# Kernel optimization log

Hardware: AMD Instinct MI355X
Metric: run time of the kernel (lower is better)

The kernel has to match this reference:

```python
import jax, jax.numpy as jnp
import numpy as np

H = 16        # attn_num
A = 64        # head dim
W = 512       # sliding-window length (ar_attn_window_len)
THETA = 10000.0
EPS = 1e-6    # norm_eps


def _rope(x):
    # x: [b, h, s, a]
    s, a = x.shape[2], x.shape[3]
    inv_freq = (1.0 / THETA) ** (jnp.arange(0, a, 2, dtype=jnp.float32) / a)
    freqs = jnp.arange(s, dtype=jnp.float32)[:, None] * inv_freq[None, :]  # [s, a/2]
    cos, sin = jnp.cos(freqs), jnp.sin(freqs)
    x1, x2 = jnp.split(x, 2, axis=-1)
    return jnp.concatenate([x1 * cos + x2 * sin, -x1 * sin + x2 * cos], axis=-1)


def _l2_normalize(x):
    # F.normalize(x, dim=-1, eps): x / max(||x||_2, eps)
    n = jnp.sqrt(jnp.sum(x * x, axis=-1, keepdims=True))
    return x / jnp.maximum(n, EPS)


def setup_inputs() -> dict:
    key = jax.random.key(0)
    kq, kk, kv = jax.random.split(key, 3)
    b, s, d = 2, 4096, H * A
    return {
        "xq": jax.random.normal(kq, (b, s, d), dtype=jnp.float32),
        "xk": jax.random.normal(kk, (b, s, d), dtype=jnp.float32),
        "xv": jax.random.normal(kv, (b, s, d), dtype=jnp.float32),
    }


def reference(xq, xk, xv):
    b, s, d = xq.shape
    to_heads = lambda x: x.reshape(b, s, H, A).transpose(0, 2, 1, 3)  # b h s a
    q, k, v = to_heads(xq), to_heads(xk), to_heads(xv)

    # qk-norm then RoPE, exactly as Attention.forward
    q = _rope(_l2_normalize(q))
    k = _rope(_l2_normalize(k))

    # Block-banded causal sliding-window attention (honors the block sparsity):
    # query block i attends only to key blocks i-1 and i (window = block size W).
    nb = s // W
    qb = q.reshape(b, H, nb, W, A)

    def band(x):
        xb = x.reshape(b, H, nb, W, A)
        xp = jnp.pad(xb, ((0, 0), (0, 0), (1, 0), (0, 0), (0, 0)))  # zero block in front
        return jnp.concatenate([xp[:, :, :-1], xp[:, :, 1:]], axis=3)  # [b,H,nb,2W,A]

    kb, vb = band(k), band(v)

    scale = 1.0 / np.sqrt(A)
    scores = jnp.einsum("bhnqa,bhnka->bhnqk", qb, kb) * scale  # [b,H,nb,W,2W]

    # mask: causal (q >= kv), window (q - kv < W), and kv index in range (>= 0)
    r = jnp.arange(W)
    c = jnp.arange(2 * W)
    diff = r[:, None] - (c[None, :] - W)               # q_global - kv_global
    within = (diff >= 0) & (diff < W)                   # [W, 2W]
    kv_global = (jnp.arange(nb)[:, None] - 1) * W + c[None, :]  # [nb, 2W]
    mask = within[None, :, :] & (kv_global[:, None, :] >= 0)    # [nb, W, 2W]

    scores = jnp.where(mask[None, None], scores, -1e30)
    p = jax.nn.softmax(scores, axis=-1)
    out = jnp.einsum("bhnqk,bhnka->bhnqa", p, vb)       # [b,H,nb,W,A]
    out = out.reshape(b, H, s, A).transpose(0, 2, 1, 3).reshape(b, s, d)
    return out
```

## Files before the change

### kernel.cpp

```cpp
#include <hip/hip_runtime.h>

#define NB 2
#define NH 16
#define SEQ 4096
#define HD 64
#define DIM 1024
#define WIN 512

typedef float f32x16 __attribute__((ext_vector_type(16)));
typedef short bf16x8 __attribute__((ext_vector_type(8)));
typedef unsigned int u32x4 __attribute__((ext_vector_type(4)));
typedef unsigned int u32x2 __attribute__((ext_vector_type(2)));
typedef unsigned short u16;
typedef unsigned int u32;

__device__ __forceinline__ u16 f2bf(float x) {
    u32 u = __float_as_uint(x);
    u += 0x7FFFu + ((u >> 16) & 1u);
    return (u16)(u >> 16);
}

__device__ __forceinline__ u32 cvtpk(float lo, float hi) {
    u32 r;
    asm("v_cvt_pk_bf16_f32 %0, %1, %2" : "=v"(r) : "v"(lo), "v"(hi));
    return r;
}

__device__ __forceinline__ float pexp2(float x) {
    return 1.f + x * (0.69314718f + x * (0.24022651f + x * 0.05550411f));
}

__global__ void trig_kernel(float* __restrict__ ct, float* __restrict__ st) {
    int idx = blockIdx.x * 256 + threadIdx.x;
    int s = idx >> 5, j = idx & 31;
    float inv = powf(1.0f / 10000.0f, (float)j * (1.0f / 32.0f));
    float ang = (float)s * inv;
    ct[idx] = cosf(ang);
    st[idx] = sinf(ang);
}

__device__ __forceinline__ void norm_rope_row(const float* __restrict__ row,
                                              const float* __restrict__ cr,
                                              const float* __restrict__ sr,
                                              float scale, u16* __restrict__ dst, int a) {
    float4 u0 = *(const float4*)(row + 8 * a);
    float4 u1 = *(const float4*)(row + 8 * a + 4);
    float4 v0 = *(const float4*)(row + 32 + 8 * a);
    float4 v1 = *(const float4*)(row + 32 + 8 * a + 4);
    float x1[8] = {u0.x, u0.y, u0.z, u0.w, u1.x, u1.y, u1.z, u1.w};
    float x2[8] = {v0.x, v0.y, v0.z, v0.w, v1.x, v1.y, v1.z, v1.w};
    float ss = 0.f;
#pragma unroll
    for (int i = 0; i < 8; ++i) ss += x1[i] * x1[i] + x2[i] * x2[i];
    ss += __shfl_xor(ss, 1);
    ss += __shfl_xor(ss, 2);
    float rn = scale / fmaxf(sqrtf(ss), 1e-6f);
    u16 o1[8], o2[8];
#pragma unroll
    for (int i = 0; i < 8; ++i) {
        float c = cr[8 * a + i], sn = sr[8 * a + i];
        o1[i] = f2bf((x1[i] * c + x2[i] * sn) * rn);
        o2[i] = f2bf((x2[i] * c - x1[i] * sn) * rn);
    }
    uint4 w1, w2;
    w1.x = (u32)o1[0] | ((u32)o1[1] << 16); w1.y = (u32)o1[2] | ((u32)o1[3] << 16);
    w1.z = (u32)o1[4] | ((u32)o1[5] << 16); w1.w = (u32)o1[6] | ((u32)o1[7] << 16);
    w2.x = (u32)o2[0] | ((u32)o2[1] << 16); w2.y = (u32)o2[2] | ((u32)o2[3] << 16);
    w2.z = (u32)o2[4] | ((u32)o2[5] << 16); w2.w = (u32)o2[6] | ((u32)o2[7] << 16);
    *(uint4*)(dst + 8 * a) = w1;
    *(uint4*)(dst + 32 + 8 * a) = w2;
}

__global__ void k_prep(const float* __restrict__ xk,
                       const float* __restrict__ ctab, const float* __restrict__ stab,
                       u16* __restrict__ Kn) {
    int bid = blockIdx.x;
    int bh = bid >> 6, stile = bid & 63;
    int b = bh >> 4, h = bh & 15;
    int t = threadIdx.x;
    int lr = t >> 2, a = t & 3;
    int s = stile * 64 + lr;
    size_t inoff = ((size_t)(b * SEQ + s)) * DIM + h * HD;
    size_t outoff = ((size_t)bh * SEQ + s) * HD;
    norm_rope_row(xk + inoff, ctab + (size_t)s * 32, stab + (size_t)s * 32, 1.0f, Kn + outoff, a);
}

__global__ void v_prep(const float* __restrict__ xv, u16* __restrict__ Vt) {
    __shared__ u16 tile[64][66];
    int bid = blockIdx.x;
    int bh = bid >> 6, stile = bid & 63;
    int b = bh >> 4, h = bh & 15;
    int t = threadIdx.x;
    int lr = t >> 2, a = t & 3;
    int s = stile * 64 + lr;
    const float* vrow = xv + ((size_t)(b * SEQ + s)) * DIM + h * HD + 16 * a;
#pragma unroll
    for (int c = 0; c < 4; ++c) {
        float4 w = *(const float4*)(vrow + 4 * c);
        tile[lr][16 * a + 4 * c + 0] = f2bf(w.x);
        tile[lr][16 * a + 4 * c + 1] = f2bf(w.y);
        tile[lr][16 * a + 4 * c + 2] = f2bf(w.z);
        tile[lr][16 * a + 4 * c + 3] = f2bf(w.w);
    }
    __syncthreads();
    int d = t >> 2;
    u32 pk[8];
#pragma unroll
    for (int i = 0; i < 8; ++i) {
        u16 lo = tile[16 * a + 2 * i][d];
        u16 hi = tile[16 * a + 2 * i + 1][d];
        pk[i] = (u32)lo | ((u32)hi << 16);
    }
    u16* dst = Vt + ((size_t)bh * HD + d) * SEQ + stile * 64 + 16 * a;
    *(uint4*)(dst) = make_uint4(pk[0], pk[1], pk[2], pk[3]);
    *(uint4*)(dst + 8) = make_uint4(pk[4], pk[5], pk[6], pk[7]);
}

#define KROW 72
#define VROW 40
__global__ __launch_bounds__(256, 4) void attn_kernel(const float* __restrict__ xq,
                                                      const u16* __restrict__ Kn,
                                                      const u16* __restrict__ Vt,
                                                      const float* __restrict__ ctab,
                                                      const float* __restrict__ stab,
                                                      float* __restrict__ out) {
    __shared__ __align__(16) u16 Kl[2][32 * KROW];
    __shared__ __align__(16) u16 Vl[2][64 * VROW];
    int phys = blockIdx.x;
    int logical = (phys & 7) * 128 + (phys >> 3);
    int bh = logical >> 5, qt = logical & 31;
    int b = bh >> 4, h = bh & 15;
    int tid = threadIdx.x;
    int w = tid >> 6, l = tid & 63;
    int q = l & 31, hi = l >> 5;
    int qblk = qt * 128;
    int qw0 = qblk + w * 32;
    const u16* Kh = Kn + (size_t)bh * SEQ * HD;
    const u16* Vh = Vt + (size_t)bh * HD * SEQ;
    int dq = qw0 + q;

    const float* qrow = xq + ((size_t)(b * SEQ + dq)) * DIM + h * HD;
    float4 xa0 = *(const float4*)(qrow + hi * 8);
    float4 xa1 = *(const float4*)(qrow + hi * 8 + 4);
    float4 xb0 = *(const float4*)(qrow + 16 + hi * 8);
    float4 xb1 = *(const float4*)(qrow + 16 + hi * 8 + 4);
    float4 ya0 = *(const float4*)(qrow + 32 + hi * 8);
    float4 ya1 = *(const float4*)(qrow + 36 + hi * 8);
    float4 yb0 = *(const float4*)(qrow + 48 + hi * 8);
    float4 yb1 = *(const float4*)(qrow + 52 + hi * 8);
    auto d4 = [](float4 v) { return v.x * v.x + v.y * v.y + v.z * v.z + v.w * v.w; };
    float ss = d4(xa0) + d4(xa1) + d4(xb0) + d4(xb1) + d4(ya0) + d4(ya1) + d4(yb0) + d4(yb1);
    ss += __shfl_xor(ss, 32);
    float rn = (0.125f * 1.44269504f) / fmaxf(sqrtf(ss), 1e-6f);
    const float* crp = ctab + (size_t)dq * 32;
    const float* srp = stab + (size_t)dq * 32;
    float4 ca0 = *(const float4*)(crp + hi * 8);
    float4 ca1 = *(const float4*)(crp + hi * 8 + 4);
    float4 cb0 = *(const float4*)(crp + 16 + hi * 8);
    float4 cb1 = *(const float4*)(crp + 16 + hi * 8 + 4);
    float4 sa0 = *(const float4*)(srp + hi * 8);
    float4 sa1 = *(const float4*)(srp + hi * 8 + 4);
    float4 sb0 = *(const float4*)(srp + 16 + hi * 8);
    float4 sb1 = *(const float4*)(srp + 16 + hi * 8 + 4);
    auto mk1 = [&](float4 x0, float4 x1f, float4 y0, float4 y1f,
                   float4 c0, float4 c1, float4 s0, float4 s1) -> bf16x8 {
        u32x4 r;
        r[0] = cvtpk((x0.x * c0.x + y0.x * s0.x) * rn, (x0.y * c0.y + y0.y * s0.y) * rn);
        r[1] = cvtpk((x0.z * c0.z + y0.z * s0.z) * rn, (x0.w * c0.w + y0.w * s0.w) * rn);
        r[2] = cvtpk((x1f.x * c1.x + y1f.x * s1.x) * rn, (x1f.y * c1.y + y1f.y * s1.y) * rn);
        r[3] = cvtpk((x1f.z * c1.z + y1f.z * s1.z) * rn, (x1f.w * c1.w + y1f.w * s1.w) * rn);
        return __builtin_bit_cast(bf16x8, r);
    };
    auto mk2 = [&](float4 x0, float4 x1f, float4 y0, float4 y1f,
                   float4 c0, float4 c1, float4 s0, float4 s1) -> bf16x8 {
        u32x4 r;
        r[0] = cvtpk((y0.x * c0.x - x0.x * s0.x) * rn, (y0.y * c0.y - x0.y * s0.y) * rn);
        r[1] = cvtpk((y0.z * c0.z - x0.z * s0.z) * rn, (y0.w * c0.w - x0.w * s0.w) * rn);
        r[2] = cvtpk((y1f.x * c1.x - x1f.x * s1.x) * rn, (y1f.y * c1.y - x1f.y * s1.y) * rn);
        r[3] = cvtpk((y1f.z * c1.z - x1f.z * s1.z) * rn, (y1f.w * c1.w - x1f.w * s1.w) * rn);
        return __builtin_bit_cast(bf16x8, r);
    };
    bf16x8 qf0 = mk1(xa0, xa1, ya0, ya1, ca0, ca1, sa0, sa1);
    bf16x8 qf1 = mk1(xb0, xb1, yb0, yb1, cb0, cb1, sb0, sb1);
    bf16x8 qf2 = mk2(xa0, xa1, ya0, ya1, ca0, ca1, sa0, sa1);
    bf16x8 qf3 = mk2(xb0, xb1, yb0, yb1, cb0, cb1, sb0, sb1);

    f32x16 acc0, acc1;
#pragma unroll
    for (int i = 0; i < 16; ++i) { acc0[i] = 0.f; acc1[i] = 0.f; }
    float l_ = 0.f;

    int tw0 = (qw0 - (WIN - 1)) >> 5; if (tw0 < 0) tw0 = 0;
    int tw1 = qw0 >> 5;
    int bt0 = (qblk - (WIN - 1)) >> 5; if (bt0 < 0) bt0 = 0;
    int bt1 = (qblk + 96) >> 5;

    int krow = tid >> 3, kc = (tid & 7) * 8;
    int vrw  = tid >> 2, vc = (tid & 3) * 8;
    const u16* kgl = Kh + (size_t)krow * HD + kc;
    const u16* vgl = Vh + (size_t)vrw * SEQ + vc;
    u16* kls0 = &Kl[0][krow * KROW + kc];
    u16* kls1 = &Kl[1][krow * KROW + kc];
    u16* vls0 = &Vl[0][vrw * VROW + vc];
    u16* vls1 = &Vl[1][vrw * VROW + vc];

    const u16* krd0 = &Kl[0][q * KROW + hi * 8];
    const u16* krd1 = &Kl[1][q * KROW + hi * 8];
    const u16* vrd0a = &Vl[0][q * VROW + hi * 8];
    const u16* vrd0b = &Vl[0][(32 + q) * VROW + hi * 8];
    const u16* vrd1a = &Vl[1][q * VROW + hi * 8];
    const u16* vrd1b = &Vl[1][(32 + q) * VROW + hi * 8];

    {
        uint4 gk = *(const uint4*)(kgl + ((size_t)bt0 << 5) * HD);
        uint4 gv = *(const uint4*)(vgl + (bt0 << 5));
        *(uint4*)kls0 = gk;
        *(uint4*)vls0 = gv;
    }
    __syncthreads();

    int c = 0;
    for (int t = bt0; t <= bt1; ++t) {
        int kv0 = t << 5;
        bool more = t < bt1;
        uint4 gk, gv;
        if (more) {
            gk = *(const uint4*)(kgl + ((size_t)(kv0 + 32)) * HD);
            gv = *(const uint4*)(vgl + (kv0 + 32));
        }

        if (t >= tw0 && t <= tw1) {
            bool mask = (t == tw0) || (t == tw1);
            const u16* kr = c ? krd1 : krd0;
            const u16* va = c ? vrd1a : vrd0a;
            const u16* vb = c ? vrd1b : vrd0b;

            bf16x8 k0 = *(const bf16x8*)(kr);
            bf16x8 k1 = *(const bf16x8*)(kr + 16);
            bf16x8 k2 = *(const bf16x8*)(kr + 32);
            bf16x8 k3 = *(const bf16x8*)(kr + 48);

            f32x16 st;
#pragma unroll
            for (int i = 0; i < 16; ++i) st[i] = 0.f;
            st = __builtin_amdgcn_mfma_f32_32x32x16_bf16(k0, qf0, st, 0, 0, 0);
            st = __builtin_amdgcn_mfma_f32_32x32x16_bf16(k1, qf1, st, 0, 0, 0);
            st = __builtin_amdgcn_mfma_f32_32x32x16_bf16(k2, qf2, st, 0, 0, 0);
            st = __builtin_amdgcn_mfma_f32_32x32x16_bf16(k3, qf3, st, 0, 0, 0);

            bf16x8 va0 = *(const bf16x8*)(va);
            bf16x8 va1 = *(const bf16x8*)(va + 16);
            bf16x8 vb0 = *(const bf16x8*)(vb);
            bf16x8 vb1 = *(const bf16x8*)(vb + 16);

            int base = dq - (kv0 + 4 * hi);
            u32 wd[8];
            float l0 = 0.f, l1 = 0.f;
#pragma unroll
            for (int i = 0; i < 8; ++i) {
                int r0 = 2 * i, r1 = 2 * i + 1;
                float e0 = pexp2(st[r0]);
                float e1 = pexp2(st[r1]);
                if (mask) {
                    int k0off = (r0 & 3) + 8 * (r0 >> 2);
                    int k1off = (r1 & 3) + 8 * (r1 >> 2);
                    e0 = ((u32)(base - k0off) < (u32)WIN) ? e0 : 0.f;
                    e1 = ((u32)(base - k1off) < (u32)WIN) ? e1 : 0.f;
                }
                l0 += e0; l1 += e1;
                wd[i] = cvtpk(e0, e1);
            }
            l_ += l0 + l1;

            u32x4 b1, b2;
#if __has_builtin(__builtin_amdgcn_permlane32_swap)
            u32x2 sA = __builtin_amdgcn_permlane32_swap(wd[0], wd[2], false, false);
            u32x2 sB = __builtin_amdgcn_permlane32_swap(wd[1], wd[3], false, false);
            u32x2 sC = __builtin_amdgcn_permlane32_swap(wd[4], wd[6], false, false);
            u32x2 sD = __builtin_amdgcn_permlane32_swap(wd[5], wd[7], false, false);
            b1 = (u32x4){ sA[0], sB[0], sA[1], sB[1] };
            b2 = (u32x4){ sC[0], sD[0], sC[1], sD[1] };
#else
            u32 e0 = __shfl_xor(hi ? wd[0] : wd[2], 32);
            u32 e1 = __shfl_xor(hi ? wd[1] : wd[3], 32);
            u32 e2 = __shfl_xor(hi ? wd[4] : wd[6], 32);
            u32 e3 = __shfl_xor(hi ? wd[5] : wd[7], 32);
            b1 = (u32x4){ hi ? e0 : wd[0], hi ? e1 : wd[1], hi ? wd[2] : e0, hi ? wd[3] : e1 };
            b2 = (u32x4){ hi ? e2 : wd[4], hi ? e3 : wd[5], hi ? wd[6] : e2, hi ? wd[7] : e3 };
#endif
            bf16x8 pb1 = __builtin_bit_cast(bf16x8, b1);
            bf16x8 pb2 = __builtin_bit_cast(bf16x8, b2);

            acc0 = __builtin_amdgcn_mfma_f32_32x32x16_bf16(va0, pb1, acc0, 0, 0, 0);
            acc0 = __builtin_amdgcn_mfma_f32_32x32x16_bf16(va1, pb2, acc0, 0, 0, 0);
            acc1 = __builtin_amdgcn_mfma_f32_32x32x16_bf16(vb0, pb1, acc1, 0, 0, 0);
            acc1 = __builtin_amdgcn_mfma_f32_32x32x16_bf16(vb1, pb2, acc1, 0, 0, 0);
        }

        if (more) {
            *(uint4*)(c ? kls0 : kls1) = gk;
            *(uint4*)(c ? vls0 : vls1) = gv;
        }
        __syncthreads();
        c ^= 1;
    }

    l_ += __shfl_xor(l_, 32);
    float inv = 1.0f / l_;
    float* orow = out + ((size_t)(b * SEQ + dq)) * DIM + h * HD;
#pragma unroll
    for (int g = 0; g < 4; ++g) {
        float4 v0 = { acc0[4 * g + 0] * inv, acc0[4 * g + 1] * inv,
                      acc0[4 * g + 2] * inv, acc0[4 * g + 3] * inv };
        float4 v1 = { acc1[4 * g + 0] * inv, acc1[4 * g + 1] * inv,
                      acc1[4 * g + 2] * inv, acc1[4 * g + 3] * inv };
        *(float4*)(orow + 8 * g + 4 * hi) = v0;
        *(float4*)(orow + 32 + 8 * g + 4 * hi) = v1;
    }
}

extern "C" void kernel_launch(void* const* d_in, const int* in_sizes, int n_in,
                              void* d_out, int out_size, void* d_ws, size_t ws_size,
                              hipStream_t stream) {
    (void)in_sizes; (void)n_in; (void)out_size; (void)ws_size;
    const float* xq = (const float*)d_in[0];
    const float* xk = (const float*)d_in[1];
    const float* xv = (const float*)d_in[2];
    float* out = (float*)d_out;

    const size_t HEADS_ELEMS = (size_t)NB * NH * SEQ * HD;
    u16* Kn = (u16*)d_ws;
    u16* Vt = Kn + HEADS_ELEMS;
    float* ctab = (float*)(Vt + HEADS_ELEMS);
    float* stab = ctab + (size_t)SEQ * 32;

    trig_kernel<<<dim3(512), dim3(256), 0, stream>>>(ctab, stab);
    k_prep<<<dim3(2048), dim3(256), 0, stream>>>(xk, ctab, stab, Kn);
    v_prep<<<dim3(2048), dim3(256), 0, stream>>>(xv, Vt);
    attn_kernel<<<dim3(1024), dim3(256), 0, stream>>>(xq, Kn, Vt, ctab, stab, out);
}
```

Measured before the change: 70.46 us.

## Deepen K/V prefetch to two tiles ahead with triple-buffered LDS

Global loads for K and V tiles are now issued two iterations ahead into alternating register sets, and LDS uses three stages instead of two. The aim is to hide more global memory latency behind the MFMA work of the current tile. In exchange it uses more registers and 50% more shared memory, which may reduce occupancy under the 256x4 launch bound, and the dynamic buffer indexing adds address arithmetic.

```diff
diff --git a/kernel.cpp b/kernel.cpp
--- a/kernel.cpp
+++ b/kernel.cpp
@@ -124,8 +124,8 @@
                                                       const float* __restrict__ ctab,
                                                       const float* __restrict__ stab,
                                                       float* __restrict__ out) {
-    __shared__ __align__(16) u16 Kl[2][32 * KROW];
-    __shared__ __align__(16) u16 Vl[2][64 * VROW];
+    __shared__ __align__(16) u16 Kl[3][32 * KROW];
+    __shared__ __align__(16) u16 Vl[3][64 * VROW];
     int phys = blockIdx.x;
     int logical = (phys & 7) * 128 + (phys >> 3);
     int bh = logical >> 5, qt = logical & 31;
@@ -199,42 +199,43 @@
     int vrw  = tid >> 2, vc = (tid & 3) * 8;
     const u16* kgl = Kh + (size_t)krow * HD + kc;
     const u16* vgl = Vh + (size_t)vrw * SEQ + vc;
-    u16* kls0 = &Kl[0][krow * KROW + kc];
-    u16* kls1 = &Kl[1][krow * KROW + kc];
-    u16* vls0 = &Vl[0][vrw * VROW + vc];
-    u16* vls1 = &Vl[1][vrw * VROW + vc];
-
-    const u16* krd0 = &Kl[0][q * KROW + hi * 8];
-    const u16* krd1 = &Kl[1][q * KROW + hi * 8];
-    const u16* vrd0a = &Vl[0][q * VROW + hi * 8];
-    const u16* vrd0b = &Vl[0][(32 + q) * VROW + hi * 8];
-    const u16* vrd1a = &Vl[1][q * VROW + hi * 8];
-    const u16* vrd1b = &Vl[1][(32 + q) * VROW + hi * 8];
-
+    int klo = krow * KROW + kc;
+    int vlo = vrw * VROW + vc;
+
+    auto issueLoad = [&](int t, uint4& gk, uint4& gv) {
+        size_t S = (size_t)t << 5;
+        gk = *(const uint4*)(kgl + S * HD);
+        gv = *(const uint4*)(vgl + S);
+    };
+    auto writeStage = [&](int buf, const uint4& gk, const uint4& gv) {
+        *(uint4*)&Kl[buf][klo] = gk;
+        *(uint4*)&Vl[buf][vlo] = gv;
+    };
+
+    uint4 gkA, gvA, gkB, gvB;
     {
-        uint4 gk = *(const uint4*)(kgl + ((size_t)bt0 << 5) * HD);
-        uint4 gv = *(const uint4*)(vgl + (bt0 << 5));
-        *(uint4*)kls0 = gk;
-        *(uint4*)vls0 = gv;
-    }
+        uint4 gk, gv;
+        issueLoad(bt0, gk, gv);
+        writeStage(0, gk, gv);
+    }
+    if (bt0 + 1 <= bt1) issueLoad(bt0 + 1, gkA, gvA);
     __syncthreads();
 
     int c = 0;
     for (int t = bt0; t <= bt1; ++t) {
-        int kv0 = t << 5;
-        bool more = t < bt1;
-        uint4 gk, gv;
-        if (more) {
-            gk = *(const uint4*)(kgl + ((size_t)(kv0 + 32)) * HD);
-            gv = *(const uint4*)(vgl + (kv0 + 32));
+        bool useA = ((t - bt0) & 1) == 0;
+        if (t + 2 <= bt1) {
+            if (useA) issueLoad(t + 2, gkB, gvB);
+            else      issueLoad(t + 2, gkA, gvA);
         }
 
         if (t >= tw0 && t <= tw1) {
+            int kv0 = t << 5;
             bool mask = (t == tw0) || (t == tw1);
-            const u16* kr = c ? krd1 : krd0;
-            const u16* va = c ? vrd1a : vrd0a;
-            const u16* vb = c ? vrd1b : vrd0b;
-
+            const u16* Kb = &Kl[c][0];
+            const u16* Vb = &Vl[c][0];
+
+            const u16* kr = Kb + q * KROW + hi * 8;
             bf16x8 k0 = *(const bf16x8*)(kr);
             bf16x8 k1 = *(const bf16x8*)(kr + 16);
             bf16x8 k2 = *(const bf16x8*)(kr + 32);
@@ -248,6 +249,8 @@
             st = __builtin_amdgcn_mfma_f32_32x32x16_bf16(k2, qf2, st, 0, 0, 0);
             st = __builtin_amdgcn_mfma_f32_32x32x16_bf16(k3, qf3, st, 0, 0, 0);
 
+            const u16* va = Vb + q * VROW + hi * 8;
+            const u16* vb = Vb + (32 + q) * VROW + hi * 8;
             bf16x8 va0 = *(const bf16x8*)(va);
             bf16x8 va1 = *(const bf16x8*)(va + 16);
             bf16x8 vb0 = *(const bf16x8*)(vb);
@@ -297,12 +300,13 @@
             acc1 = __builtin_amdgcn_mfma_f32_32x32x16_bf16(vb1, pb2, acc1, 0, 0, 0);
         }
 
-        if (more) {
-            *(uint4*)(c ? kls0 : kls1) = gk;
-            *(uint4*)(c ? vls0 : vls1) = gv;
+        if (t + 1 <= bt1) {
+            int nc = c + 1; if (nc == 3) nc = 0;
+            if (useA) writeStage(nc, gkA, gvA);
+            else      writeStage(nc, gkB, gvB);
         }
         __syncthreads();
-        c ^= 1;
+        c = (c + 1 == 3) ? 0 : c + 1;
     }
 
     l_ += __shfl_xor(l_, 32);
```

New measurement: 76.44 us. 8.5% more time.
